# Kernel optimization log

Measured on AMD Instinct MI355X. Metric: run time of the kernel, lower is better.

Reference implementation:

```python
import jax, jax.numpy as jnp
import numpy as np

HEADS = 4

def _conv1x1(x, w, b):
    # x: [B,C,H,W], w: [O,C], b: [O]
    return jnp.einsum('bchw,oc->bohw', x, w) + b[None, :, None, None]

def _dwconv(x, w, b, pad):
    # x: [B,C,H,W], w: [C,1,kh,kw] depthwise
    out = jax.lax.conv_general_dilated(
        x, w, window_strides=(1, 1), padding=[(pad, pad), (pad, pad)],
        dimension_numbers=('NCHW', 'OIHW', 'NCHW'), feature_group_count=x.shape[1])
    if b is not None:
        out = out + b[None, :, None, None]
    return out

def _l2norm(x, axis=-1, eps=1e-12):
    n = jnp.sqrt(jnp.sum(x * x, axis=axis, keepdims=True))
    return x / jnp.maximum(n, eps)

def setup_inputs() -> dict:
    key = jax.random.key(0)
    ks = jax.random.split(key, 16)
    B, H, W, C = 2, 256, 256, 64
    s = 0.02
    inp = {
        'x_in': jax.random.normal(ks[0], (B, H, W, C), jnp.float32),
        'mask': jax.random.uniform(ks[1], (B, H, W, C), jnp.float32),
        'Wq': jax.random.normal(ks[2], (C, C), jnp.float32) * s,
        'Wk': jax.random.normal(ks[3], (C, C), jnp.float32) * s,
        'Wv': jax.random.normal(ks[4], (C, C), jnp.float32) * s,
        'rescale': jnp.ones((HEADS, 1, 1), jnp.float32),
        'Wp': jax.random.normal(ks[5], (C, C), jnp.float32) * s,
        'bp': jnp.zeros((C,), jnp.float32),
        'mm_w1': jax.random.normal(ks[6], (C, C), jnp.float32) * s,
        'mm_b1': jnp.zeros((C,), jnp.float32),
        'mm_w2': jax.random.normal(ks[7], (C, C), jnp.float32) * s,
        'mm_b2': jnp.zeros((C,), jnp.float32),
        'mm_dw': jax.random.normal(ks[8], (C, 1, 5, 5), jnp.float32) * s,
        'mm_dwb': jnp.zeros((C,), jnp.float32),
        'pe_w1': jax.random.normal(ks[9], (C, 1, 3, 3), jnp.float32) * s,
        'pe_w2': jax.random.normal(ks[10], (C, 1, 3, 3), jnp.float32) * s,
    }
    return inp

def reference(x_in, mask, Wq, Wk, Wv, rescale, Wp, bp,
              mm_w1, mm_b1, mm_w2, mm_b2, mm_dw, mm_dwb, pe_w1, pe_w2):
    b, h, w, c = x_in.shape
    heads = HEADS
    d = c // heads
    n = h * w
    x = x_in.reshape(b, n, c)

    def to_heads(t):  # [b,n,c] -> [b,heads,n,d]
        return t.reshape(b, n, heads, d).transpose(0, 2, 1, 3)

    # torch Linear: y = x @ W^T
    q = to_heads(jnp.einsum('bnc,oc->bno', x, Wq))
    k = to_heads(jnp.einsum('bnc,oc->bno', x, Wk))
    v = to_heads(jnp.einsum('bnc,oc->bno', x, Wv))

    # MaskGuidedMechanism
    m = mask.transpose(0, 3, 1, 2)          # [b,c,h,w]
    m1 = _conv1x1(m, mm_w1, mm_b1)
    attn_map = jax.nn.sigmoid(_dwconv(_conv1x1(m1, mm_w2, mm_b2), mm_dw, mm_dwb, 2))
    ma = m1 * attn_map + m1                  # [b,c,h,w]
    ma = to_heads(ma.transpose(0, 2, 3, 1).reshape(b, n, c))

    v = v * ma

    # transpose to channel-attention layout: [b,heads,d,n]
    q, k, v = (t.transpose(0, 1, 3, 2) for t in (q, k, v))
    q = _l2norm(q, axis=-1)
    k = _l2norm(k, axis=-1)

    attn = jnp.einsum('bhdn,bhen->bhde', k, q) * rescale[None]  # [b,heads,d,d]
    attn = jax.nn.softmax(attn, axis=-1)
    out = jnp.einsum('bhde,bhen->bhdn', attn, v)                # [b,heads,d,n]

    out = out.transpose(0, 3, 1, 2).reshape(b, n, heads * d)    # [b,n,c]
    out_c = (jnp.einsum('bnc,oc->bno', out, Wp) + bp).reshape(b, h, w, c)

    xp = x_in.transpose(0, 3, 1, 2)
    pe = _dwconv(jax.nn.gelu(_dwconv(xp, pe_w1, None, 1), approximate=False), pe_w2, None, 1)
    out_p = pe.transpose(0, 2, 3, 1)

    return out_c + out_p
```

## Files before the change

kernel.cpp:

```cpp
#include <hip/hip_runtime.h>
#include <hip/hip_bf16.h>
#include <math.h>

#define BB 2
#define NPIX 131072

#define WS_G    0
#define WS_SSQ  8192
#define WS_M    9216
#define WS_WSWZ_BYTE ((size_t)17408*4)
#define WS_M2_BYTE   (WS_WSWZ_BYTE + 40960)

typedef __attribute__((ext_vector_type(8))) short short8;
typedef __attribute__((ext_vector_type(4))) float f32x4;

__device__ __forceinline__ unsigned short f2bf(float f) {
    unsigned u = __float_as_uint(f);
    u += 0x7FFFu + ((u >> 16) & 1u);
    return (unsigned short)(u >> 16);
}
__device__ __forceinline__ float bf2f(unsigned short s) {
    return __uint_as_float((unsigned)s << 16);
}
__device__ __forceinline__ void lds_fence() {
    __asm__ __volatile__("s_waitcnt lgkmcnt(0)" ::: "memory");
}
__device__ __forceinline__ float fast_sigmoid(float a) {
    return __builtin_amdgcn_rcpf(1.f + __expf(-a));
}
__device__ __forceinline__ float fast_gelu(float x) {
    float y = 1.5957691216057308f * fmaf(0.044715f * x, x * x, x);
    return x * fast_sigmoid(y);
}

__global__ __launch_bounds__(256) void k_prep(const float* __restrict__ Wq,
    const float* __restrict__ Wk, const float* __restrict__ Wv,
    const float* __restrict__ w1, const float* __restrict__ w2,
    unsigned short* __restrict__ wg, float* __restrict__ ws)
{
    const int i = blockIdx.x*256 + threadIdx.x;
    if (i < 9216) ws[i] = 0.f;
    const int f = i >> 9, l = (i >> 3) & 63, j = i & 7;
    const int matot = f >> 1, kh = f & 1;
    const int mat = matot >> 2, ot = matot & 3;
    const int o = ot*16 + (l & 15);
    const int cc = kh*32 + ((l >> 4) & 3)*8 + j;
    const float* Wsrc[5] = {Wq, Wk, Wv, w1, w2};
    wg[i] = f2bf(Wsrc[mat][o*64 + cc]);
}

__global__ __launch_bounds__(256, 2) void k_fused(
    const float* __restrict__ x, const float* __restrict__ mask,
    const unsigned short* __restrict__ wg,
    const float* __restrict__ b1, const float* __restrict__ b2,
    float* __restrict__ ws, float* __restrict__ out,
    __hip_bfloat16* __restrict__ m2out)
{
    __shared__ unsigned short wswz[20480];
    __shared__ unsigned short scr[4][3264];
    __shared__ float s_ssq[4][2][4][64];
    const int tid = threadIdx.x, lane = tid & 63, w = tid >> 6;
    const int quad = lane >> 4, col = lane & 15;
    const int blk = blockIdx.x, b = blk >> 8, slot = blk & 3;

    for (int i = tid; i < 2560; i += 256)
        ((uint4*)wswz)[i] = ((const uint4*)wg)[i];
    __syncthreads();

    float b1v[4], b2v[4];
#pragma unroll
    for (int ot = 0; ot < 4; ++ot) {
        b1v[ot] = b1[ot*16 + col];
        b2v[ot] = b2[ot*16 + col];
    }

#define WFRAG(matot, kh) (*(const short8*)&wswz[(((matot)*2 + (kh))*64 + lane)*8])

    f32x4 gacc[4];
#pragma unroll
    for (int h = 0; h < 4; ++h) gacc[h] = (f32x4){0.f, 0.f, 0.f, 0.f};
    float ssq[2][4];
#pragma unroll
    for (int mm = 0; mm < 2; ++mm)
#pragma unroll
        for (int ot = 0; ot < 4; ++ot) ssq[mm][ot] = 0.f;
    const short8 z8 = {0,0,0,0,0,0,0,0};
    unsigned short* S  = scr[w];
    unsigned short* S2 = scr[w] + 2112;

    for (int t = 0; t < 4; ++t) {
        const int pbase = blk*256 + t*64 + w*16;

        short8 xA[2], mA[2];
        {
            const float* xs = x    + ((size_t)(pbase + col))*64 + quad*8;
            const float* ms = mask + ((size_t)(pbase + col))*64 + quad*8;
#pragma unroll
            for (int kh = 0; kh < 2; ++kh) {
                float4 a0 = *(const float4*)(xs + kh*32);
                float4 a1 = *(const float4*)(xs + kh*32 + 4);
                float4 b0 = *(const float4*)(ms + kh*32);
                float4 b1f = *(const float4*)(ms + kh*32 + 4);
#pragma unroll
                for (int j = 0; j < 4; ++j) {
                    xA[kh][j]   = (short)f2bf((&a0.x)[j]);
                    xA[kh][4+j] = (short)f2bf((&a1.x)[j]);
                    mA[kh][j]   = (short)f2bf((&b0.x)[j]);
                    mA[kh][4+j] = (short)f2bf((&b1f.x)[j]);
                }
            }
        }

#pragma unroll
        for (int mm = 0; mm < 2; ++mm) {
#pragma unroll
            for (int ot = 0; ot < 4; ++ot) {
                f32x4 a = {0.f, 0.f, 0.f, 0.f};
                a = __builtin_amdgcn_mfma_f32_16x16x32_bf16(xA[0], WFRAG(mm*4+ot,0), a, 0,0,0);
                a = __builtin_amdgcn_mfma_f32_16x16x32_bf16(xA[1], WFRAG(mm*4+ot,1), a, 0,0,0);
#pragma unroll
                for (int r = 0; r < 4; ++r) {
                    S[mm*1536 + (ot*16 + col)*24 + quad*4 + r] = f2bf(a[r]);
                    ssq[mm][ot] = fmaf(a[r], a[r], ssq[mm][ot]);
                }
            }
        }
        __builtin_amdgcn_wave_barrier();

        {
            const int gb = (quad & 1) * 8;
#pragma unroll
            for (int h = 0; h < 4; ++h) {
                short8 aq = *(const short8*)&S[(h*16 + col)*24 + gb];
                short8 ak = *(const short8*)&S[1536 + (h*16 + col)*24 + gb];
                if (quad >= 2) { aq = z8; ak = z8; }
                gacc[h] = __builtin_amdgcn_mfma_f32_16x16x32_bf16(ak, aq, gacc[h], 0,0,0);
            }
        }
        lds_fence();

        f32x4 vfr[4], m1fr[4];
#pragma unroll
        for (int ot = 0; ot < 4; ++ot) {
            f32x4 a = {0.f, 0.f, 0.f, 0.f};
            a = __builtin_amdgcn_mfma_f32_16x16x32_bf16(xA[0], WFRAG(8+ot,0), a, 0,0,0);
            a = __builtin_amdgcn_mfma_f32_16x16x32_bf16(xA[1], WFRAG(8+ot,1), a, 0,0,0);
            vfr[ot] = a;
        }
#pragma unroll
        for (int ot = 0; ot < 4; ++ot) {
            f32x4 a = {0.f, 0.f, 0.f, 0.f};
            a = __builtin_amdgcn_mfma_f32_16x16x32_bf16(mA[0], WFRAG(12+ot,0), a, 0,0,0);
            a = __builtin_amdgcn_mfma_f32_16x16x32_bf16(mA[1], WFRAG(12+ot,1), a, 0,0,0);
#pragma unroll
            for (int r = 0; r < 4; ++r) a[r] += b1v[ot];
            m1fr[ot] = a;
        }

        float* vscr = (float*)S;
#pragma unroll
        for (int ot = 0; ot < 4; ++ot)
#pragma unroll
            for (int r = 0; r < 4; ++r)
                vscr[(quad*4+r)*66 + ot*16 + col] = vfr[ot][r] * m1fr[ot][r];
        __builtin_amdgcn_wave_barrier();
        {
            const int rb = lane >> 5, ci = (lane & 31)*2;
#pragma unroll
            for (int pp = 0; pp < 8; ++pp) {
                const int row = pp*2 + rb;
                float2 v2 = *(const float2*)&vscr[row*66 + ci];
                *(float2*)&out[((size_t)(pbase + row))*64 + ci] = v2;
            }
        }

#pragma unroll
        for (int ot = 0; ot < 4; ++ot)
#pragma unroll
            for (int r = 0; r < 4; ++r)
                S2[(quad*4+r)*72 + ot*16 + col] = f2bf(m1fr[ot][r]);
        __builtin_amdgcn_wave_barrier();
        short8 a2[2];
#pragma unroll
        for (int kh = 0; kh < 2; ++kh)
            a2[kh] = *(const short8*)&S2[col*72 + kh*32 + quad*8];
        lds_fence();

#pragma unroll
        for (int ot = 0; ot < 4; ++ot) {
            f32x4 a = {0.f, 0.f, 0.f, 0.f};
            a = __builtin_amdgcn_mfma_f32_16x16x32_bf16(a2[0], WFRAG(16+ot,0), a, 0,0,0);
            a = __builtin_amdgcn_mfma_f32_16x16x32_bf16(a2[1], WFRAG(16+ot,1), a, 0,0,0);
#pragma unroll
            for (int r = 0; r < 4; ++r)
                S2[(quad*4+r)*72 + ot*16 + col] = f2bf(a[r] + b2v[ot]);
        }
        __builtin_amdgcn_wave_barrier();
        {
            unsigned short* m2u = (unsigned short*)m2out;
            const int rb = lane >> 5, ci = (lane & 31)*2;
#pragma unroll
            for (int pp = 0; pp < 8; ++pp) {
                const int row = pp*2 + rb;
                unsigned vv = *(const unsigned*)&S2[row*72 + ci];
                *(unsigned*)&m2u[((size_t)(pbase + row))*64 + ci] = vv;
            }
        }
        lds_fence();
    }

    __syncthreads();

    float* gr = (float*)&scr[0][0];
    if (w < 2) {
#pragma unroll
        for (int h = 0; h < 4; ++h)
#pragma unroll
            for (int r = 0; r < 4; ++r)
                gr[w*1024 + (h*16 + quad*4 + r)*16 + col] = gacc[h][r];
    }
#pragma unroll
    for (int mm = 0; mm < 2; ++mm)
#pragma unroll
        for (int ot = 0; ot < 4; ++ot)
            s_ssq[w][mm][ot][lane] = ssq[mm][ot];
    __syncthreads();
    if (w >= 2) {
#pragma unroll
        for (int h = 0; h < 4; ++h)
#pragma unroll
            for (int r = 0; r < 4; ++r)
                gr[(w-2)*1024 + (h*16 + quad*4 + r)*16 + col] += gacc[h][r];
    }
    __syncthreads();
    float* Gg = ws + WS_G + (size_t)slot*2048 + (size_t)b*1024;
    for (int idx = tid; idx < 1024; idx += 256)
        atomicAdd(&Gg[idx], gr[idx] + gr[1024 + idx]);
    if (tid < 128) {
        const int which = tid >> 6, cidx = tid & 63;
        const int ot = cidx >> 4, cl = cidx & 15;
        float s = 0.f;
#pragma unroll
        for (int wv = 0; wv < 4; ++wv)
#pragma unroll
            for (int q = 0; q < 4; ++q)
                s += s_ssq[wv][which][ot][q*16 + cl];
        atomicAdd(ws + WS_SSQ + (size_t)slot*256 + which*128 + b*64 + cidx, s);
    }
#undef WFRAG
}

__global__ __launch_bounds__(256) void k_attn(const float* __restrict__ rescale,
    const float* __restrict__ Wp, float* __restrict__ ws)
{
    __shared__ float sAtt[1024];
    const int b = blockIdx.x, t = threadIdx.x;
    const int d = t >> 4, e = t & 15;
#pragma unroll
    for (int h = 0; h < 4; ++h) {
        float g = 0.f, nk2 = 0.f, nq2 = 0.f;
#pragma unroll
        for (int s = 0; s < 4; ++s) {
            g   += ws[WS_G + s*2048 + b*1024 + (h*16+d)*16 + e];
            nk2 += ws[WS_SSQ + s*256 + 128 + b*64 + h*16 + d];
            nq2 += ws[WS_SSQ + s*256 +   0 + b*64 + h*16 + e];
        }
        float nk = fmaxf(sqrtf(nk2), 1e-12f);
        float nq = fmaxf(sqrtf(nq2), 1e-12f);
        float val = g / (nk*nq) * rescale[h];
        float m = val;
        for (int off = 1; off < 16; off <<= 1) m = fmaxf(m, __shfl_xor(m, off, 16));
        float ev = expf(val - m);
        float s2 = ev;
        for (int off = 1; off < 16; off <<= 1) s2 += __shfl_xor(s2, off, 16);
        sAtt[h*256 + d*16 + e] = ev / s2;
    }
    __syncthreads();
    unsigned short* Mtw = (unsigned short*)(ws + WS_M) + (size_t)b*4096;
    for (int i = t; i < 4096; i += 256) {
        const int f = i >> 9, l = (i >> 3) & 63, j = i & 7;
        const int ot = f >> 1, kh = f & 1;
        const int o = ot*16 + (l & 15);
        const int cc = kh*32 + ((l >> 4) & 3)*8 + j;
        const int h = cc >> 4, ee = cc & 15;
        float acc = 0.f;
#pragma unroll
        for (int d2 = 0; d2 < 16; ++d2)
            acc = fmaf(Wp[o*64 + h*16 + d2], sAtt[h*256 + d2*16 + ee], acc);
        Mtw[i] = f2bf(acc);
    }
}

__global__ __launch_bounds__(256, 4) void k_fp(
    const float* __restrict__ x, const __hip_bfloat16* __restrict__ m2g,
    const float* __restrict__ wsM, const float* __restrict__ bp,
    const float* __restrict__ dw, const float* __restrict__ dwb,
    const float* __restrict__ pw1, const float* __restrict__ pw2,
    float* __restrict__ out)
{
    __shared__ __align__(16) char smem[31232];
    unsigned short* xt  = (unsigned short*)smem;
    unsigned short* t1  = (unsigned short*)(smem + 18432);
    unsigned short* m2s = (unsigned short*)smem;
    unsigned short* vmL = (unsigned short*)(smem + 18432);
    unsigned short* peL = (unsigned short*)smem;
    const int tid = threadIdx.x, lane = tid & 63, w = tid >> 6;
    const int quad = lane >> 4, col = lane & 15;
    const int bid = blockIdx.x;
    const int b = bid >> 10, tile = bid & 1023;
    const int y0 = (tile >> 5) * 8, x0 = (tile & 31) * 8;
    const int c = lane;

    float w1r[9], w2r[9];
#pragma unroll
    for (int k = 0; k < 9; ++k) { w1r[k] = pw1[c*9+k]; w2r[k] = pw2[c*9+k]; }

    for (int i = tid; i < 12*12*64; i += 256) {
        int yy = i / 768, xx = (i % 768) >> 6;
        int gy = y0 + yy - 2, gx = x0 + xx - 2;
        float v = 0.f;
        if (gy >= 0 && gy < 256 && gx >= 0 && gx < 256)
            v = x[(((size_t)b*256 + gy)*256 + gx)*64 + c];
        xt[i] = f2bf(v);
    }
    __syncthreads();
    for (int i = tid; i < 10*10*64; i += 256) {
        int yy = i / 640, xx = (i % 640) >> 6;
        int gy = y0 + yy - 1, gx = x0 + xx - 1;
        float val = 0.f;
        if (gy >= 0 && gy < 256 && gx >= 0 && gx < 256) {
            float acc = 0.f;
#pragma unroll
            for (int ky = 0; ky < 3; ++ky)
#pragma unroll
                for (int kx = 0; kx < 3; ++kx)
                    acc = fmaf(bf2f(xt[((yy+ky)*12 + xx+kx)*64 + c]),
                               w1r[ky*3+kx], acc);
            val = fast_gelu(acc);
        }
        t1[i] = f2bf(val);
    }
    __syncthreads();

    unsigned peP[4][2];
#pragma unroll
    for (int g = 0; g < 4; ++g) {
        const int p0 = w*16 + g*4, py = p0 >> 3, px0 = p0 & 7;
#pragma unroll
        for (int j2 = 0; j2 < 2; ++j2) {
            unsigned pk = 0;
#pragma unroll
            for (int jj = 0; jj < 2; ++jj) {
                const int j = j2*2 + jj;
                float acc = 0.f;
#pragma unroll
                for (int ky = 0; ky < 3; ++ky)
#pragma unroll
                    for (int kx = 0; kx < 3; ++kx)
                        acc = fmaf(bf2f(t1[((py+ky)*10 + px0+j+kx)*64 + c]),
                                   w2r[ky*3+kx], acc);
                pk |= (unsigned)f2bf(acc) << (jj*16);
            }
            peP[g][j2] = pk;
        }
    }
    __syncthreads();

    for (int i2 = tid; i2 < 2304; i2 += 256) {
        const int pos = i2 >> 4, c4 = (i2 & 15) * 4;
        const int yy = pos / 12, xx = pos - yy*12;
        const int gy = y0 + yy - 2, gx = x0 + xx - 2;
        ushort4 us = make_ushort4(0, 0, 0, 0);
        if (gy >= 0 && gy < 256 && gx >= 0 && gx < 256)
            us = *(const ushort4*)&m2g[(((size_t)b*256 + gy)*256 + gx)*64 + c4];
        *(ushort4*)&m2s[pos*64 + c4] = us;
    }
    __syncthreads();

    const float dwbr = dwb[c];
    float dwr[25];
#pragma unroll
    for (int k = 0; k < 25; ++k) dwr[k] = dw[c*25+k];

#pragma unroll
    for (int g = 0; g < 4; ++g) {
        const int p0 = w*16 + g*4;
        const int py = p0 >> 3, px0 = p0 & 7;
        float acc[4] = {dwbr, dwbr, dwbr, dwbr};
#pragma unroll
        for (int ky = 0; ky < 5; ++ky) {
            const int rbase = ((py+ky)*12 + px0)*64 + c;
#pragma unroll
            for (int kx8 = 0; kx8 < 8; ++kx8) {
                const float tv = bf2f(m2s[rbase + kx8*64]);
#pragma unroll
                for (int j = 0; j < 4; ++j) {
                    const int kk = kx8 - j;
                    if (kk >= 0 && kk < 5)
                        acc[j] = fmaf(tv, dwr[ky*5 + kk], acc[j]);
                }
            }
        }
#pragma unroll
        for (int j = 0; j < 4; ++j) {
            const size_t P = (size_t)b*65536 + (size_t)(y0+py)*256 + (x0+px0+j);
            const float s = fast_sigmoid(acc[j]);
            vmL[(p0 + j)*72 + c] = f2bf(out[P*64 + c] * (1.f + s));
        }
    }
    __syncthreads();

#pragma unroll
    for (int g = 0; g < 4; ++g)
#pragma unroll
        for (int j = 0; j < 4; ++j)
            peL[(w*16 + g*4 + j)*72 + c] =
                (unsigned short)(peP[g][j >> 1] >> ((j & 1)*16));
    __builtin_amdgcn_wave_barrier();
    lds_fence();

    short8 aV[2];
#pragma unroll
    for (int kh = 0; kh < 2; ++kh)
        aV[kh] = *(const short8*)&vmL[(w*16 + col)*72 + kh*32 + quad*8];
    float bpv[4];
#pragma unroll
    for (int ot = 0; ot < 4; ++ot) bpv[ot] = bp[ot*16 + col];

    const unsigned short* Mtw = (const unsigned short*)wsM + (size_t)b*4096;
#pragma unroll
    for (int ot = 0; ot < 4; ++ot) {
        short8 m0 = *(const short8*)&Mtw[((ot*2+0)*64 + lane)*8];
        short8 m1f = *(const short8*)&Mtw[((ot*2+1)*64 + lane)*8];
        f32x4 a = {0.f, 0.f, 0.f, 0.f};
        a = __builtin_amdgcn_mfma_f32_16x16x32_bf16(aV[0], m0, a, 0,0,0);
        a = __builtin_amdgcn_mfma_f32_16x16x32_bf16(aV[1], m1f, a, 0,0,0);
#pragma unroll
        for (int r = 0; r < 4; ++r) {
            const int pl = w*16 + quad*4 + r;
            const int gy = y0 + (pl >> 3), gx = x0 + (pl & 7);
            out[(((size_t)b*256 + gy)*256 + gx)*64 + ot*16 + col] =
                a[r] + bpv[ot] + bf2f(peL[pl*72 + ot*16 + col]);
        }
    }
}

extern "C" void kernel_launch(void* const* d_in, const int* in_sizes, int n_in,
                              void* d_out, int out_size, void* d_ws, size_t ws_size,
                              hipStream_t stream)
{
    const float* x    = (const float*)d_in[0];
    const float* mask = (const float*)d_in[1];
    const float* Wq   = (const float*)d_in[2];
    const float* Wk   = (const float*)d_in[3];
    const float* Wv   = (const float*)d_in[4];
    const float* resc = (const float*)d_in[5];
    const float* Wp   = (const float*)d_in[6];
    const float* bp   = (const float*)d_in[7];
    const float* mw1  = (const float*)d_in[8];
    const float* mb1  = (const float*)d_in[9];
    const float* mw2  = (const float*)d_in[10];
    const float* mb2  = (const float*)d_in[11];
    const float* mdw  = (const float*)d_in[12];
    const float* mdwb = (const float*)d_in[13];
    const float* pw1  = (const float*)d_in[14];
    const float* pw2  = (const float*)d_in[15];
    float* ws  = (float*)d_ws;
    unsigned short* wg = (unsigned short*)((char*)d_ws + WS_WSWZ_BYTE);
    __hip_bfloat16* m2 = (__hip_bfloat16*)((char*)d_ws + WS_M2_BYTE);
    float* out = (float*)d_out;

    k_prep <<<80,   256, 0, stream>>>(Wq, Wk, Wv, mw1, mw2, wg, ws);
    k_fused<<<512,  256, 0, stream>>>(x, mask, wg, mb1, mb2, ws, out, m2);
    k_attn <<<2,    256, 0, stream>>>(resc, Wp, ws);
    k_fp   <<<2048, 256, 0, stream>>>(x, m2, ws + WS_M, bp, mdw, mdwb,
                                      pw1, pw2, out);
}
```

Baseline: 215.4 us.

## Drop prep kernel, replace atomics with per-block partials, store v*m1 as fp16

Removes the k_prep launch by having each k_fused block convert and swizzle the weights to bf16 itself. Gram and sum-of-squares atomics into four slots become plain per-block partial writes, which k_attn then reduces over 256 blocks per batch. The intermediate v*m1 stored in the output buffer is now packed as fp16 rather than fp32, halving that traffic, and the x halo load in k_fp is vectorised to float4. The costs are a serial 256-step reduction in a 2-block k_attn, redundant weight conversion in every k_fused block, and fp16 precision loss on the intermediate.

```diff
diff --git a/kernel.cpp b/kernel.cpp
--- a/kernel.cpp
+++ b/kernel.cpp
@@ -1,15 +1,15 @@
 #include <hip/hip_runtime.h>
 #include <hip/hip_bf16.h>
+#include <hip/hip_fp16.h>
 #include <math.h>
 
 #define BB 2
 #define NPIX 131072
 
-#define WS_G    0
-#define WS_SSQ  8192
-#define WS_M    9216
-#define WS_WSWZ_BYTE ((size_t)17408*4)
-#define WS_M2_BYTE   (WS_WSWZ_BYTE + 40960)
+#define WS_GP 0
+#define WS_SP 524288
+#define WS_M  589824
+#define WS_M2_BYTE ((size_t)589824*4 + 16384)
 
 typedef __attribute__((ext_vector_type(8))) short short8;
 typedef __attribute__((ext_vector_type(4))) float f32x4;
@@ -33,25 +33,11 @@
     return x * fast_sigmoid(y);
 }
 
-__global__ __launch_bounds__(256) void k_prep(const float* __restrict__ Wq,
-    const float* __restrict__ Wk, const float* __restrict__ Wv,
-    const float* __restrict__ w1, const float* __restrict__ w2,
-    unsigned short* __restrict__ wg, float* __restrict__ ws)
-{
-    const int i = blockIdx.x*256 + threadIdx.x;
-    if (i < 9216) ws[i] = 0.f;
-    const int f = i >> 9, l = (i >> 3) & 63, j = i & 7;
-    const int matot = f >> 1, kh = f & 1;
-    const int mat = matot >> 2, ot = matot & 3;
-    const int o = ot*16 + (l & 15);
-    const int cc = kh*32 + ((l >> 4) & 3)*8 + j;
-    const float* Wsrc[5] = {Wq, Wk, Wv, w1, w2};
-    wg[i] = f2bf(Wsrc[mat][o*64 + cc]);
-}
-
 __global__ __launch_bounds__(256, 2) void k_fused(
     const float* __restrict__ x, const float* __restrict__ mask,
-    const unsigned short* __restrict__ wg,
+    const float* __restrict__ Wq, const float* __restrict__ Wk,
+    const float* __restrict__ Wv, const float* __restrict__ w1,
+    const float* __restrict__ w2,
     const float* __restrict__ b1, const float* __restrict__ b2,
     float* __restrict__ ws, float* __restrict__ out,
     __hip_bfloat16* __restrict__ m2out)
@@ -61,10 +47,27 @@
     __shared__ float s_ssq[4][2][4][64];
     const int tid = threadIdx.x, lane = tid & 63, w = tid >> 6;
     const int quad = lane >> 4, col = lane & 15;
-    const int blk = blockIdx.x, b = blk >> 8, slot = blk & 3;
-
-    for (int i = tid; i < 2560; i += 256)
-        ((uint4*)wswz)[i] = ((const uint4*)wg)[i];
+    const int blk = blockIdx.x;
+
+    for (int i = tid; i < 2560; i += 256) {
+        const int f = i >> 6, l = i & 63;
+        const int matot = f >> 1, kh = f & 1;
+        const int mat = matot >> 2, ot = matot & 3;
+        const float* Wm = (mat == 0) ? Wq : (mat == 1) ? Wk :
+                          (mat == 2) ? Wv : (mat == 3) ? w1 : w2;
+        const int o = ot*16 + (l & 15);
+        const int cc = kh*32 + ((l >> 4) & 3)*8;
+        const float* src = Wm + o*64 + cc;
+        float4 a0 = *(const float4*)src;
+        float4 a1 = *(const float4*)(src + 4);
+        short8 s8;
+#pragma unroll
+        for (int j = 0; j < 4; ++j) {
+            s8[j]   = (short)f2bf((&a0.x)[j]);
+            s8[4+j] = (short)f2bf((&a1.x)[j]);
+        }
+        *(short8*)&wswz[(size_t)i*8] = s8;
+    }
     __syncthreads();
 
     float b1v[4], b2v[4];
@@ -165,12 +168,15 @@
                 vscr[(quad*4+r)*66 + ot*16 + col] = vfr[ot][r] * m1fr[ot][r];
         __builtin_amdgcn_wave_barrier();
         {
+            unsigned short* o16 = (unsigned short*)out;
             const int rb = lane >> 5, ci = (lane & 31)*2;
 #pragma unroll
             for (int pp = 0; pp < 8; ++pp) {
                 const int row = pp*2 + rb;
                 float2 v2 = *(const float2*)&vscr[row*66 + ci];
-                *(float2*)&out[((size_t)(pbase + row))*64 + ci] = v2;
+                unsigned pk = (unsigned)__half_as_ushort(__float2half(v2.x))
+                            | ((unsigned)__half_as_ushort(__float2half(v2.y)) << 16);
+                *(unsigned*)&o16[((size_t)(pbase + row))*128 + ci] = pk;
             }
         }
 
@@ -233,9 +239,9 @@
                 gr[(w-2)*1024 + (h*16 + quad*4 + r)*16 + col] += gacc[h][r];
     }
     __syncthreads();
-    float* Gg = ws + WS_G + (size_t)slot*2048 + (size_t)b*1024;
+    float* Gp = ws + WS_GP + (size_t)blk*1024;
     for (int idx = tid; idx < 1024; idx += 256)
-        atomicAdd(&Gg[idx], gr[idx] + gr[1024 + idx]);
+        Gp[idx] = gr[idx] + gr[1024 + idx];
     if (tid < 128) {
         const int which = tid >> 6, cidx = tid & 63;
         const int ot = cidx >> 4, cl = cidx & 15;
@@ -245,7 +251,7 @@
 #pragma unroll
             for (int q = 0; q < 4; ++q)
                 s += s_ssq[wv][which][ot][q*16 + cl];
-        atomicAdd(ws + WS_SSQ + (size_t)slot*256 + which*128 + b*64 + cidx, s);
+        ws[WS_SP + (size_t)blk*128 + which*64 + cidx] = s;
     }
 #undef WFRAG
 }
@@ -253,18 +259,31 @@
 __global__ __launch_bounds__(256) void k_attn(const float* __restrict__ rescale,
     const float* __restrict__ Wp, float* __restrict__ ws)
 {
+    __shared__ float sG[1024];
+    __shared__ float sS[128];
     __shared__ float sAtt[1024];
     const int b = blockIdx.x, t = threadIdx.x;
     const int d = t >> 4, e = t & 15;
+
+    for (int idx = t; idx < 1024; idx += 256) {
+        float s = 0.f;
+        const float* p = ws + WS_GP + (size_t)(b*256)*1024 + idx;
+        for (int j = 0; j < 256; ++j) s += p[(size_t)j*1024];
+        sG[idx] = s;
+    }
+    if (t < 128) {
+        float s = 0.f;
+        const float* p = ws + WS_SP + (size_t)(b*256)*128 + t;
+        for (int j = 0; j < 256; ++j) s += p[(size_t)j*128];
+        sS[t] = s;
+    }
+    __syncthreads();
+
 #pragma unroll
     for (int h = 0; h < 4; ++h) {
-        float g = 0.f, nk2 = 0.f, nq2 = 0.f;
-#pragma unroll
-        for (int s = 0; s < 4; ++s) {
-            g   += ws[WS_G + s*2048 + b*1024 + (h*16+d)*16 + e];
-            nk2 += ws[WS_SSQ + s*256 + 128 + b*64 + h*16 + d];
-            nq2 += ws[WS_SSQ + s*256 +   0 + b*64 + h*16 + e];
-        }
+        float g   = sG[(h*16 + d)*16 + e];
+        float nk2 = sS[64 + h*16 + d];
+        float nq2 = sS[ 0 + h*16 + e];
         float nk = fmaxf(sqrtf(nk2), 1e-12f);
         float nq = fmaxf(sqrtf(nq2), 1e-12f);
         float val = g / (nk*nq) * rescale[h];
@@ -315,13 +334,16 @@
 #pragma unroll
     for (int k = 0; k < 9; ++k) { w1r[k] = pw1[c*9+k]; w2r[k] = pw2[c*9+k]; }
 
-    for (int i = tid; i < 12*12*64; i += 256) {
-        int yy = i / 768, xx = (i % 768) >> 6;
-        int gy = y0 + yy - 2, gx = x0 + xx - 2;
-        float v = 0.f;
+    for (int i = tid; i < 2304; i += 256) {
+        const int pos = i >> 4, c4 = (i & 15) * 4;
+        const int yy = pos / 12, xx = pos - yy*12;
+        const int gy = y0 + yy - 2, gx = x0 + xx - 2;
+        float4 v = {0.f, 0.f, 0.f, 0.f};
         if (gy >= 0 && gy < 256 && gx >= 0 && gx < 256)
-            v = x[(((size_t)b*256 + gy)*256 + gx)*64 + c];
-        xt[i] = f2bf(v);
+            v = *(const float4*)&x[(((size_t)b*256 + gy)*256 + gx)*64 + c4];
+        ushort4 us;
+        us.x = f2bf(v.x); us.y = f2bf(v.y); us.z = f2bf(v.z); us.w = f2bf(v.w);
+        *(ushort4*)&xt[pos*64 + c4] = us;
     }
     __syncthreads();
     for (int i = tid; i < 10*10*64; i += 256) {
@@ -382,6 +404,7 @@
 #pragma unroll
     for (int k = 0; k < 25; ++k) dwr[k] = dw[c*25+k];
 
+    const unsigned short* o16 = (const unsigned short*)out;
 #pragma unroll
     for (int g = 0; g < 4; ++g) {
         const int p0 = w*16 + g*4;
@@ -405,7 +428,8 @@
         for (int j = 0; j < 4; ++j) {
             const size_t P = (size_t)b*65536 + (size_t)(y0+py)*256 + (x0+px0+j);
             const float s = fast_sigmoid(acc[j]);
-            vmL[(p0 + j)*72 + c] = f2bf(out[P*64 + c] * (1.f + s));
+            const float vm0 = __half2float(__ushort_as_half(o16[P*128 + c]));
+            vmL[(p0 + j)*72 + c] = f2bf(vm0 * (1.f + s));
         }
     }
     __syncthreads();
@@ -466,12 +490,11 @@
     const float* pw1  = (const float*)d_in[14];
     const float* pw2  = (const float*)d_in[15];
     float* ws  = (float*)d_ws;
-    unsigned short* wg = (unsigned short*)((char*)d_ws + WS_WSWZ_BYTE);
     __hip_bfloat16* m2 = (__hip_bfloat16*)((char*)d_ws + WS_M2_BYTE);
     float* out = (float*)d_out;
 
-    k_prep <<<80,   256, 0, stream>>>(Wq, Wk, Wv, mw1, mw2, wg, ws);
-    k_fused<<<512,  256, 0, stream>>>(x, mask, wg, mb1, mb2, ws, out, m2);
+    k_fused<<<512,  256, 0, stream>>>(x, mask, Wq, Wk, Wv, mw1, mw2,
+                                      mb1, mb2, ws, out, m2);
     k_attn <<<2,    256, 0, stream>>>(resc, Wp, ws);
     k_fp   <<<2048, 256, 0, stream>>>(x, m2, ws + WS_M, bp, mdw, mdwb,
                                       pw1, pw2, out);
```

Result: slower. 243.6 us (+13.1%).
